# Kernel optimization log

Hardware: AMD Instinct MI355X
Metric: run time of the kernel (lower is better)

Reference implementation:

```python
import jax, jax.numpy as jnp
import numpy as np

NUM_SEQS = 128
TOTAL_TOKENS = 65536
HIDDEN = 768
FF = 3072
EPS = 1e-12  # torch F.normalize default eps


def _make_prompt_lens(rng: np.random.Generator) -> np.ndarray:
    # Ragged lengths in [64, 960], adjusted so they sum exactly to TOTAL_TOKENS.
    lens = rng.integers(64, 960, size=NUM_SEQS).astype(np.int64)
    lens = np.maximum(1, (lens * (TOTAL_TOKENS / lens.sum())).astype(np.int64))
    lens[-1] += TOTAL_TOKENS - lens.sum()
    assert lens.sum() == TOTAL_TOKENS and (lens > 0).all()
    return lens


def setup_inputs() -> dict:
    key = jax.random.key(0)
    k1, k2, k3 = jax.random.split(key, 3)
    hidden_states = jax.random.normal(k1, (TOTAL_TOKENS, HIDDEN), dtype=jnp.float32)
    prompt_lens = jnp.asarray(_make_prompt_lens(np.random.default_rng(0)))
    W1 = jax.random.normal(k2, (FF, HIDDEN), dtype=jnp.float32) * (HIDDEN ** -0.5)
    W2 = jax.random.normal(k3, (HIDDEN, FF), dtype=jnp.float32) * (FF ** -0.5)
    return {"hidden_states": hidden_states, "prompt_lens": prompt_lens, "W1": W1, "W2": W2}


def reference(hidden_states, prompt_lens, W1, W2):
    # hidden_states: [T, H]; prompt_lens: [S] summing to T.
    T = hidden_states.shape[0]
    S = prompt_lens.shape[0]
    # segment id of each token: index of first cumsum strictly greater than position
    seg_ids = jnp.searchsorted(jnp.cumsum(prompt_lens), jnp.arange(T), side="right")
    sums = jax.ops.segment_sum(hidden_states, seg_ids, num_segments=S)  # [S, H]
    pooled = sums / prompt_lens[:, None].astype(hidden_states.dtype)     # mean pool
    h = jnp.einsum("sh,fh->sf", pooled, W1)   # dense1: 768 -> 3072 (no bias)
    h = jnp.einsum("sf,hf->sh", h, W2)        # dense2: 3072 -> 768 (no bias)
    norm = jnp.linalg.norm(h, ord=2, axis=-1, keepdims=True)
    return h / jnp.maximum(norm, EPS)         # L2 normalize, [S, H]
```

## Files before the change

kernel.cpp:

```cpp
#include <hip/hip_runtime.h>

#define TOK   65536
#define HID   768
#define NSEQ  128
#define FFD   3072
#define PCH   32
#define NPCH  (TOK / PCH)
#define KS1   8
#define KCH1  96
#define KS2   24
#define KCH2  128

__device__ __forceinline__ void add4(float4& a, const float4 b) {
  a.x += b.x; a.y += b.y; a.z += b.z; a.w += b.w;
}

__global__ __launch_bounds__(192, 6) void pool_kernel(
    const float* __restrict__ x, const int* __restrict__ lens,
    float* __restrict__ pooled) {
  __shared__ int sc[NSEQ];
  const int tid = threadIdx.x;
  if (tid < NSEQ) sc[tid] = lens[tid];
  __syncthreads();
  for (int off = 1; off < NSEQ; off <<= 1) {
    int v = 0;
    if (tid < NSEQ && tid >= off) v = sc[tid - off];
    __syncthreads();
    if (tid < NSEQ) sc[tid] += v;
    __syncthreads();
  }
  const int t0 = blockIdx.x * PCH;
  int lo = 0, hi = NSEQ - 1;
  while (lo < hi) { int mid = (lo + hi) >> 1; if (sc[mid] <= t0) lo = mid + 1; else hi = mid; }
  const int seg = lo;
  const int segend = sc[seg];
  const int segstart = seg ? sc[seg - 1] : 0;
  const float4* p = (const float4*)x + (size_t)t0 * (HID / 4) + tid;

  if (segend >= t0 + PCH) {
    float4 a0 = make_float4(0.f,0.f,0.f,0.f), a1 = a0, a2 = a0, a3 = a0;
    #pragma unroll
    for (int i = 0; i < PCH; i += 4) {
      add4(a0, p[(size_t)(i+0) * (HID/4)]);
      add4(a1, p[(size_t)(i+1) * (HID/4)]);
      add4(a2, p[(size_t)(i+2) * (HID/4)]);
      add4(a3, p[(size_t)(i+3) * (HID/4)]);
    }
    add4(a0, a1); add4(a2, a3); add4(a0, a2);
    const float inv = 1.0f / (float)(segend - segstart);
    float* dst = pooled + (size_t)seg * HID + tid * 4;
    atomicAdd(dst + 0, a0.x * inv);
    atomicAdd(dst + 1, a0.y * inv);
    atomicAdd(dst + 2, a0.z * inv);
    atomicAdd(dst + 3, a0.w * inv);
  } else {
    const int n0 = segend - t0;
    float4 a0 = make_float4(0.f,0.f,0.f,0.f), a1 = a0;
    for (int i = 0; i < n0; ++i)  add4(a0, p[(size_t)i * (HID/4)]);
    for (int i = n0; i < PCH; ++i) add4(a1, p[(size_t)i * (HID/4)]);
    const float inv0 = 1.0f / (float)(segend - segstart);
    const float inv1 = 1.0f / (float)(sc[seg + 1] - segend);
    float* d0 = pooled + (size_t)seg * HID + tid * 4;
    atomicAdd(d0 + 0, a0.x * inv0);
    atomicAdd(d0 + 1, a0.y * inv0);
    atomicAdd(d0 + 2, a0.z * inv0);
    atomicAdd(d0 + 3, a0.w * inv0);
    float* d1 = pooled + (size_t)(seg + 1) * HID + tid * 4;
    atomicAdd(d1 + 0, a1.x * inv1);
    atomicAdd(d1 + 1, a1.y * inv1);
    atomicAdd(d1 + 2, a1.z * inv1);
    atomicAdd(d1 + 3, a1.w * inv1);
  }
}

__global__ __launch_bounds__(256) void gemm_nt(
    const float* __restrict__ A, const float* __restrict__ B,
    float* __restrict__ Cp, int N, int Kt, int kch) {
  __shared__ float As[16][132];
  __shared__ float Bs[16][36];

  const int tid = threadIdx.x;
  const int f0 = blockIdx.x * 32;
  const int k0 = blockIdx.y * kch;
  float* C = Cp + (size_t)blockIdx.y * NSEQ * N;
  const int fx = (tid & 7) * 4;
  const int sy = (tid >> 3) * 4;

  float acc[4][4];
  #pragma unroll
  for (int i = 0; i < 4; ++i)
    #pragma unroll
    for (int j = 0; j < 4; ++j) acc[i][j] = 0.f;

  for (int kc = k0; kc < k0 + kch; kc += 16) {
    #pragma unroll
    for (int r = 0; r < 2; ++r) {
      const int l = tid + 256 * r;
      const int s = l >> 2, k4 = (l & 3) * 4;
      const float4 v = *(const float4*)(A + (size_t)s * Kt + kc + k4);
      As[k4 + 0][s] = v.x; As[k4 + 1][s] = v.y;
      As[k4 + 2][s] = v.z; As[k4 + 3][s] = v.w;
    }
    if (tid < 128) {
      const int f = tid >> 2, k4 = (tid & 3) * 4;
      const float4 v = *(const float4*)(B + (size_t)(f0 + f) * Kt + kc + k4);
      Bs[k4 + 0][f] = v.x; Bs[k4 + 1][f] = v.y;
      Bs[k4 + 2][f] = v.z; Bs[k4 + 3][f] = v.w;
    }
    __syncthreads();
    #pragma unroll
    for (int kk = 0; kk < 16; ++kk) {
      const float4 aa = *(const float4*)&As[kk][sy];
      const float4 bb = *(const float4*)&Bs[kk][fx];
      acc[0][0] += aa.x*bb.x; acc[0][1] += aa.x*bb.y; acc[0][2] += aa.x*bb.z; acc[0][3] += aa.x*bb.w;
      acc[1][0] += aa.y*bb.x; acc[1][1] += aa.y*bb.y; acc[1][2] += aa.y*bb.z; acc[1][3] += aa.y*bb.w;
      acc[2][0] += aa.z*bb.x; acc[2][1] += aa.z*bb.y; acc[2][2] += aa.z*bb.z; acc[2][3] += aa.z*bb.w;
      acc[3][0] += aa.w*bb.x; acc[3][1] += aa.w*bb.y; acc[3][2] += aa.w*bb.z; acc[3][3] += aa.w*bb.w;
    }
    __syncthreads();
  }
  #pragma unroll
  for (int i = 0; i < 4; ++i)
    *(float4*)(C + (size_t)(sy + i) * N + f0 + fx) =
        make_float4(acc[i][0], acc[i][1], acc[i][2], acc[i][3]);
}

__global__ __launch_bounds__(256) void reduce_h1(
    const float* __restrict__ h1p, float* __restrict__ h1) {
  const size_t i = (size_t)blockIdx.x * 256 + threadIdx.x;
  const float4* src = (const float4*)h1p;
  float4 a = src[i];
  #pragma unroll
  for (int p = 1; p < KS1; ++p) add4(a, src[i + (size_t)p * (NSEQ * FFD / 4)]);
  ((float4*)h1)[i] = a;
}

__global__ __launch_bounds__(256) void norm_kernel(
    const float* __restrict__ outp, float* __restrict__ out) {
  const int s = blockIdx.x;
  const int tid = threadIdx.x;
  float v[3];
  #pragma unroll
  for (int j = 0; j < 3; ++j) {
    const int c = tid + 256 * j;
    float a = 0.f;
    for (int p = 0; p < KS2; ++p) a += outp[((size_t)p * NSEQ + s) * HID + c];
    v[j] = a;
  }
  float ss = v[0]*v[0] + v[1]*v[1] + v[2]*v[2];
  #pragma unroll
  for (int off = 32; off > 0; off >>= 1) ss += __shfl_down(ss, off, 64);
  __shared__ float wsum[4];
  if ((tid & 63) == 0) wsum[tid >> 6] = ss;
  __syncthreads();
  const float tot = wsum[0] + wsum[1] + wsum[2] + wsum[3];
  const float scale = 1.0f / fmaxf(sqrtf(tot), 1e-12f);
  #pragma unroll
  for (int j = 0; j < 3; ++j) out[(size_t)s * HID + tid + 256 * j] = v[j] * scale;
}

extern "C" void kernel_launch(void* const* d_in, const int* in_sizes, int n_in,
                              void* d_out, int out_size, void* d_ws, size_t ws_size,
                              hipStream_t stream) {
  const float* x    = (const float*)d_in[0];
  const int*   lens = (const int*)d_in[1];
  const float* W1   = (const float*)d_in[2];
  const float* W2   = (const float*)d_in[3];
  float* out = (float*)d_out;

  float* pooled = (float*)d_ws;
  float* h1p    = pooled + NSEQ * HID;
  float* h1     = h1p + (size_t)KS1 * NSEQ * FFD;
  float* outp   = h1 + NSEQ * FFD;

  hipMemsetAsync(pooled, 0, (size_t)NSEQ * HID * sizeof(float), stream);

  pool_kernel<<<NPCH, 192, 0, stream>>>(x, lens, pooled);
  gemm_nt<<<dim3(FFD / 32, KS1), 256, 0, stream>>>(pooled, W1, h1p, FFD, HID, KCH1);
  reduce_h1<<<NSEQ * FFD / 4 / 256, 256, 0, stream>>>(h1p, h1);
  gemm_nt<<<dim3(HID / 32, KS2), 256, 0, stream>>>(h1, W2, outp, HID, FFD, KCH2);
  norm_kernel<<<NSEQ, 256, 0, stream>>>(outp, out);
}
```

Baseline: 337.6 us.

## Replace atomic pooling with two-pass partial sums and prefetch GEMM tiles

```diff
diff --git a/kernel.cpp b/kernel.cpp
--- a/kernel.cpp
+++ b/kernel.cpp
@@ -8,18 +8,14 @@
 #define NPCH  (TOK / PCH)
 #define KS1   8
 #define KCH1  96
-#define KS2   24
-#define KCH2  128
+#define KS2   32
+#define KCH2  96
 
 __device__ __forceinline__ void add4(float4& a, const float4 b) {
   a.x += b.x; a.y += b.y; a.z += b.z; a.w += b.w;
 }
 
-__global__ __launch_bounds__(192, 6) void pool_kernel(
-    const float* __restrict__ x, const int* __restrict__ lens,
-    float* __restrict__ pooled) {
-  __shared__ int sc[NSEQ];
-  const int tid = threadIdx.x;
+__device__ __forceinline__ void scan_lens(const int* __restrict__ lens, int* sc, int tid) {
   if (tid < NSEQ) sc[tid] = lens[tid];
   __syncthreads();
   for (int off = 1; off < NSEQ; off <<= 1) {
@@ -29,13 +25,20 @@
     if (tid < NSEQ) sc[tid] += v;
     __syncthreads();
   }
+}
+
+__global__ __launch_bounds__(192, 6) void pool_part(
+    const float* __restrict__ x, const int* __restrict__ lens,
+    float* __restrict__ plo, float* __restrict__ phi) {
+  __shared__ int sc[NSEQ];
+  const int tid = threadIdx.x;
+  scan_lens(lens, sc, tid);
   const int t0 = blockIdx.x * PCH;
   int lo = 0, hi = NSEQ - 1;
   while (lo < hi) { int mid = (lo + hi) >> 1; if (sc[mid] <= t0) lo = mid + 1; else hi = mid; }
-  const int seg = lo;
-  const int segend = sc[seg];
-  const int segstart = seg ? sc[seg - 1] : 0;
+  const int segend = sc[lo];
   const float4* p = (const float4*)x + (size_t)t0 * (HID / 4) + tid;
+  float4* dlo = (float4*)plo + (size_t)blockIdx.x * (HID / 4) + tid;
 
   if (segend >= t0 + PCH) {
     float4 a0 = make_float4(0.f,0.f,0.f,0.f), a1 = a0, a2 = a0, a3 = a0;
@@ -47,30 +50,38 @@
       add4(a3, p[(size_t)(i+3) * (HID/4)]);
     }
     add4(a0, a1); add4(a2, a3); add4(a0, a2);
-    const float inv = 1.0f / (float)(segend - segstart);
-    float* dst = pooled + (size_t)seg * HID + tid * 4;
-    atomicAdd(dst + 0, a0.x * inv);
-    atomicAdd(dst + 1, a0.y * inv);
-    atomicAdd(dst + 2, a0.z * inv);
-    atomicAdd(dst + 3, a0.w * inv);
+    *dlo = a0;
   } else {
     const int n0 = segend - t0;
     float4 a0 = make_float4(0.f,0.f,0.f,0.f), a1 = a0;
-    for (int i = 0; i < n0; ++i)  add4(a0, p[(size_t)i * (HID/4)]);
+    for (int i = 0;  i < n0;  ++i) add4(a0, p[(size_t)i * (HID/4)]);
     for (int i = n0; i < PCH; ++i) add4(a1, p[(size_t)i * (HID/4)]);
-    const float inv0 = 1.0f / (float)(segend - segstart);
-    const float inv1 = 1.0f / (float)(sc[seg + 1] - segend);
-    float* d0 = pooled + (size_t)seg * HID + tid * 4;
-    atomicAdd(d0 + 0, a0.x * inv0);
-    atomicAdd(d0 + 1, a0.y * inv0);
-    atomicAdd(d0 + 2, a0.z * inv0);
-    atomicAdd(d0 + 3, a0.w * inv0);
-    float* d1 = pooled + (size_t)(seg + 1) * HID + tid * 4;
-    atomicAdd(d1 + 0, a1.x * inv1);
-    atomicAdd(d1 + 1, a1.y * inv1);
-    atomicAdd(d1 + 2, a1.z * inv1);
-    atomicAdd(d1 + 3, a1.w * inv1);
-  }
+    *dlo = a0;
+    *((float4*)phi + (size_t)blockIdx.x * (HID/4) + tid) = a1;
+  }
+}
+
+__global__ __launch_bounds__(192) void pool_reduce(
+    const int* __restrict__ lens, const float* __restrict__ plo,
+    const float* __restrict__ phi, float* __restrict__ pooled) {
+  __shared__ int sc[NSEQ];
+  const int tid = threadIdx.x;
+  scan_lens(lens, sc, tid);
+  const int s = blockIdx.x;
+  const int st = s ? sc[s - 1] : 0;
+  const int en = sc[s];
+  const int c0 = st >> 5, c1 = (en - 1) >> 5;
+  const float4* lo4 = (const float4*)plo;
+  const float4* hi4 = (const float4*)phi;
+  float4 acc = make_float4(0.f,0.f,0.f,0.f);
+  for (int c = c0; c <= c1; ++c) {
+    const float4* src = (c == c0 && (st & (PCH - 1))) ? hi4 : lo4;
+    add4(acc, src[(size_t)c * (HID / 4) + tid]);
+  }
+  const float inv = 1.0f / (float)(en - st);
+  float4 r;
+  r.x = acc.x * inv; r.y = acc.y * inv; r.z = acc.z * inv; r.w = acc.w * inv;
+  ((float4*)pooled)[(size_t)s * (HID / 4) + tid] = r;
 }
 
 __global__ __launch_bounds__(256) void gemm_nt(
@@ -85,6 +96,18 @@
   float* C = Cp + (size_t)blockIdx.y * NSEQ * N;
   const int fx = (tid & 7) * 4;
   const int sy = (tid >> 3) * 4;
+  const int sA = tid >> 2;
+  const int kA = (tid & 3) * 4;
+  const int fB = tid >> 2;
+
+  const float* pA0 = A + (size_t)sA * Kt + k0 + kA;
+  const float* pA1 = pA0 + (size_t)64 * Kt;
+  const float* pB  = B + (size_t)(f0 + fB) * Kt + k0 + kA;
+
+  float4 va0 = *(const float4*)pA0;
+  float4 va1 = *(const float4*)pA1;
+  float4 vb = make_float4(0.f,0.f,0.f,0.f);
+  if (tid < 128) vb = *(const float4*)pB;
 
   float acc[4][4];
   #pragma unroll
@@ -92,22 +115,22 @@
     #pragma unroll
     for (int j = 0; j < 4; ++j) acc[i][j] = 0.f;
 
-  for (int kc = k0; kc < k0 + kch; kc += 16) {
-    #pragma unroll
-    for (int r = 0; r < 2; ++r) {
-      const int l = tid + 256 * r;
-      const int s = l >> 2, k4 = (l & 3) * 4;
-      const float4 v = *(const float4*)(A + (size_t)s * Kt + kc + k4);
-      As[k4 + 0][s] = v.x; As[k4 + 1][s] = v.y;
-      As[k4 + 2][s] = v.z; As[k4 + 3][s] = v.w;
-    }
+  const int nch = kch >> 4;
+  for (int c = 0; c < nch; ++c) {
+    As[kA + 0][sA]      = va0.x; As[kA + 1][sA]      = va0.y;
+    As[kA + 2][sA]      = va0.z; As[kA + 3][sA]      = va0.w;
+    As[kA + 0][sA + 64] = va1.x; As[kA + 1][sA + 64] = va1.y;
+    As[kA + 2][sA + 64] = va1.z; As[kA + 3][sA + 64] = va1.w;
     if (tid < 128) {
-      const int f = tid >> 2, k4 = (tid & 3) * 4;
-      const float4 v = *(const float4*)(B + (size_t)(f0 + f) * Kt + kc + k4);
-      Bs[k4 + 0][f] = v.x; Bs[k4 + 1][f] = v.y;
-      Bs[k4 + 2][f] = v.z; Bs[k4 + 3][f] = v.w;
-    }
-    __syncthreads();
+      Bs[kA + 0][fB] = vb.x; Bs[kA + 1][fB] = vb.y;
+      Bs[kA + 2][fB] = vb.z; Bs[kA + 3][fB] = vb.w;
+    }
+    __syncthreads();
+    if (c + 1 < nch) {
+      va0 = *(const float4*)(pA0 + (c + 1) * 16);
+      va1 = *(const float4*)(pA1 + (c + 1) * 16);
+      if (tid < 128) vb = *(const float4*)(pB + (c + 1) * 16);
+    }
     #pragma unroll
     for (int kk = 0; kk < 16; ++kk) {
       const float4 aa = *(const float4*)&As[kk][sy];
@@ -144,6 +167,7 @@
   for (int j = 0; j < 3; ++j) {
     const int c = tid + 256 * j;
     float a = 0.f;
+    #pragma unroll
     for (int p = 0; p < KS2; ++p) a += outp[((size_t)p * NSEQ + s) * HID + c];
     v[j] = a;
   }
@@ -168,14 +192,15 @@
   const float* W2   = (const float*)d_in[3];
   float* out = (float*)d_out;
 
-  float* pooled = (float*)d_ws;
-  float* h1p    = pooled + NSEQ * HID;
+  float* plo    = (float*)d_ws;
+  float* phi    = plo + (size_t)NPCH * HID;
+  float* pooled = phi + (size_t)NPCH * HID;
+  float* h1p    = pooled + (size_t)NSEQ * HID;
   float* h1     = h1p + (size_t)KS1 * NSEQ * FFD;
-  float* outp   = h1 + NSEQ * FFD;
-
-  hipMemsetAsync(pooled, 0, (size_t)NSEQ * HID * sizeof(float), stream);
-
-  pool_kernel<<<NPCH, 192, 0, stream>>>(x, lens, pooled);
+  float* outp   = h1 + (size_t)NSEQ * FFD;
+
+  pool_part<<<NPCH, 192, 0, stream>>>(x, lens, plo, phi);
+  pool_reduce<<<NSEQ, 192, 0, stream>>>(lens, plo, phi, pooled);
   gemm_nt<<<dim3(FFD / 32, KS1), 256, 0, stream>>>(pooled, W1, h1p, FFD, HID, KCH1);
   reduce_h1<<<NSEQ * FFD / 4 / 256, 256, 0, stream>>>(h1p, h1);
   gemm_nt<<<dim3(HID / 32, KS2), 256, 0, stream>>>(h1, W2, outp, HID, FFD, KCH2);
```

Result: slower. 345.7 us (+2.4%).
